# Performance work log

Hardware: AMD Instinct MI355X
Metric: run time of the kernel (lower is better)

Reference implementation:

```python
import jax, jax.numpy as jnp
import numpy as np

POOL = 4      # pool_size
SR = 2        # sampling_ratio (fixed; torchvision adaptive default approximated)
C_IN = 1024
C1, C2 = 256, 128
OUT_DIM = 2048


def setup_inputs() -> dict:
    key = jax.random.key(0)
    ks = jax.random.split(key, 10)
    B, C, H, W = 8, C_IN, 64, 64
    N = 64
    x = jax.random.normal(ks[0], (B, C, H, W), dtype=jnp.float32)
    # boxes in image pixel coords (image is H*16 = 1024 px)
    img = 1024.0
    x1 = jax.random.uniform(ks[1], (B, N), minval=0.0, maxval=img - 260.0)
    y1 = jax.random.uniform(ks[2], (B, N), minval=0.0, maxval=img - 260.0)
    bw = jax.random.uniform(ks[3], (B, N), minval=32.0, maxval=256.0)
    bh = jax.random.uniform(ks[4], (B, N), minval=32.0, maxval=256.0)
    boxes = jnp.stack([x1, y1, x1 + bw, y1 + bh], axis=-1)  # [B,N,4]
    scale = jnp.float32(1.0 / 16.0)
    # detector params
    w1 = jax.random.normal(ks[5], (C1, C_IN), dtype=jnp.float32) / np.sqrt(C_IN)
    b1 = jnp.zeros((C1,), dtype=jnp.float32)
    w2 = jax.random.normal(ks[6], (C2, C1), dtype=jnp.float32) / np.sqrt(C1)
    b2 = jnp.zeros((C2,), dtype=jnp.float32)
    wl = jax.random.normal(ks[7], (OUT_DIM, C2 * POOL * POOL), dtype=jnp.float32) / np.sqrt(C2 * POOL * POOL)
    bl = jnp.zeros((OUT_DIM,), dtype=jnp.float32)
    return {"x": x, "boxes": boxes, "scale": scale,
            "w1": w1, "b1": b1, "w2": w2, "b2": b2, "wl": wl, "bl": bl}


def _axis_coords(start, size, H):
    # start,size: [R]; returns coords [R, POOL*SR], valid mask, int low/high, lerp wts
    bin_sz = size / POOL                       # [R]
    j = jnp.arange(POOL * SR, dtype=jnp.float32)
    off = jnp.floor(j / SR) + ((j % SR) + 0.5) / SR   # [P]
    c = start[:, None] + off[None, :] * bin_sz[:, None]  # [R,P]
    valid = (c >= -1.0) & (c <= H)
    c = jnp.clip(c, 0.0, H - 1.0)
    lo = jnp.floor(c).astype(jnp.int32)
    lo = jnp.minimum(lo, H - 1)
    hi = jnp.minimum(lo + 1, H - 1)
    frac = c - lo.astype(c.dtype)
    return valid, lo, hi, frac


def _roi_align(feat, boxes, scale):
    # feat: [B,C,H,W], boxes: [B,N,4] -> pooled [B*N, C, POOL, POOL]
    B, C, H, W = feat.shape
    N = boxes.shape[1]
    R = B * N
    bx = (boxes.reshape(R, 4) * scale)
    x1, y1, x2, y2 = bx[:, 0], bx[:, 1], bx[:, 2], bx[:, 3]
    rw = jnp.maximum(x2 - x1, 1.0)
    rh = jnp.maximum(y2 - y1, 1.0)
    vy, y_lo, y_hi, ly = _axis_coords(y1, rh, H)   # [R,P]
    vx, x_lo, x_hi, lx = _axis_coords(x1, rw, W)
    hy, hx = 1.0 - ly, 1.0 - lx
    bidx = jnp.repeat(jnp.arange(B, dtype=jnp.int32), N)  # [R]
    b = bidx[:, None, None]
    # gather 4 corners -> [R,P,P,C]
    v00 = feat[b, :, y_lo[:, :, None], x_lo[:, None, :]]
    v01 = feat[b, :, y_lo[:, :, None], x_hi[:, None, :]]
    v10 = feat[b, :, y_hi[:, :, None], x_lo[:, None, :]]
    v11 = feat[b, :, y_hi[:, :, None], x_hi[:, None, :]]
    w00 = (hy[:, :, None] * hx[:, None, :])[..., None]
    w01 = (hy[:, :, None] * lx[:, None, :])[..., None]
    w10 = (ly[:, :, None] * hx[:, None, :])[..., None]
    w11 = (ly[:, :, None] * lx[:, None, :])[..., None]
    val = v00 * w00 + v01 * w01 + v10 * w10 + v11 * w11
    mask = (vy[:, :, None] & vx[:, None, :])[..., None]
    val = jnp.where(mask, val, 0.0)            # [R,P,P,C]
    val = val.reshape(R, POOL, SR, POOL, SR, C).mean(axis=(2, 4))  # [R,POOL,POOL,C]
    return jnp.transpose(val, (0, 3, 1, 2))    # [R,C,POOL,POOL]


def reference(x, boxes, scale, w1, b1, w2, b2, wl, bl):
    pooled = _roi_align(x, boxes, scale)                  # [R,C,4,4]
    h = jax.nn.elu(jnp.einsum('rchw,oc->rohw', pooled, w1) + b1[None, :, None, None])
    h = jax.nn.elu(jnp.einsum('rchw,oc->rohw', h, w2) + b2[None, :, None, None])
    h = h.reshape(h.shape[0], -1)                         # [R, 128*16], torch Flatten order
    out = jax.nn.elu(h @ wl.T + bl)                       # [R, 2048]
    return out
```

## Files before the change

kernel.cpp:

```cpp
#include <hip/hip_runtime.h>
#include <math.h>

#define C_INK   1024
#define C1D     256
#define C2D     128
#define OUTD    2048
#define R_ROI   512
#define M1D     8192
#define MPIX    32768

typedef _Float16 half8 __attribute__((ext_vector_type(8)));
typedef float    f32x4 __attribute__((ext_vector_type(4)));

__device__ __forceinline__ unsigned int pack2h(float a, float b) {
    union { _Float16 h[2]; unsigned int u; } p;
    p.h[0] = (_Float16)a; p.h[1] = (_Float16)b;
    return p.u;
}
__device__ __forceinline__ float eluf(float v) { return v > 0.f ? v : expf(v) - 1.f; }

__device__ __forceinline__ half8* ldsp(_Float16* base, int row, int ch) {
    return reinterpret_cast<half8*>(base) + row * 8 + (ch ^ (row & 7));
}

__global__ __launch_bounds__(256) void cvt_weights(
    const float* __restrict__ s1, _Float16* __restrict__ d1, int n1,
    const float* __restrict__ s2, _Float16* __restrict__ d2, int n2,
    const float* __restrict__ s3, _Float16* __restrict__ d3, int n3)
{
    int i = (blockIdx.x * 256 + threadIdx.x) * 4;
    const float* s; _Float16* d;
    if (i < n1)            { s = s1; d = d1; }
    else if (i < n1 + n2)  { s = s2; d = d2; i -= n1; }
    else                   { s = s3; d = d3; i -= n1 + n2; if (i >= n3) return; }
    const float4 v = *reinterpret_cast<const float4*>(s + i);
    uint2 u; u.x = pack2h(v.x, v.y); u.y = pack2h(v.z, v.w);
    *reinterpret_cast<uint2*>(d + i) = u;
}

__global__ __launch_bounds__(512) void conv1x1_f16(
    const float* __restrict__ x, const _Float16* __restrict__ w1h,
    _Float16* __restrict__ z)
{
    __shared__ __align__(16) _Float16 As[128 * 64];
    __shared__ __align__(16) _Float16 Bs[256 * 64];

    const int tid  = threadIdx.x;
    const int lane = tid & 63;
    const int wave = tid >> 6;
    const int wr   = wave >> 2;
    const int wc   = wave & 3;
    const int m0   = blockIdx.x * 128;
    const int b    = m0 >> 12;
    const int p0   = m0 & 4095;

    const int akg = wave;
    const int bc  = tid & 7;
    const int br0 = tid >> 3;

    float ar[16];
    half8 brg[4];
    f32x4 acc[4][4];
    #pragma unroll
    for (int i = 0; i < 4; ++i)
        #pragma unroll
        for (int j = 0; j < 4; ++j) acc[i][j] = (f32x4){0.f, 0.f, 0.f, 0.f};

    const float* xbase = x + (size_t)b * C_INK * 4096 + p0;

    auto LOADT = [&](int k0) {
        const float* xk = xbase + (size_t)(k0 + akg * 8) * 4096;
        #pragma unroll
        for (int j = 0; j < 8; ++j) {
            ar[j]     = xk[j * 4096 + lane];
            ar[8 + j] = xk[j * 4096 + lane + 64];
        }
        #pragma unroll
        for (int i = 0; i < 4; ++i)
            brg[i] = *reinterpret_cast<const half8*>(
                &w1h[(size_t)(br0 + i * 64) * C_INK + k0 + bc * 8]);
    };
    auto WRITET = [&]() {
        #pragma unroll
        for (int q = 0; q < 2; ++q) {
            union { half8 h; unsigned int u[4]; } pk;
            #pragma unroll
            for (int j = 0; j < 4; ++j) pk.u[j] = pack2h(ar[q * 8 + 2 * j], ar[q * 8 + 2 * j + 1]);
            *ldsp(As, lane + q * 64, akg) = pk.h;
        }
        #pragma unroll
        for (int i = 0; i < 4; ++i) *ldsp(Bs, br0 + i * 64, bc) = brg[i];
    };
    auto COMPUTET = [&]() {
        #pragma unroll
        for (int kk = 0; kk < 2; ++kk) {
            const int ch = kk * 4 + (lane >> 4);
            half8 af[4], bf[4];
            #pragma unroll
            for (int mi = 0; mi < 4; ++mi) af[mi] = *ldsp(As, wr * 64 + mi * 16 + (lane & 15), ch);
            #pragma unroll
            for (int ni = 0; ni < 4; ++ni) bf[ni] = *ldsp(Bs, wc * 64 + ni * 16 + (lane & 15), ch);
            #pragma unroll
            for (int mi = 0; mi < 4; ++mi)
                #pragma unroll
                for (int ni = 0; ni < 4; ++ni)
                    acc[mi][ni] = __builtin_amdgcn_mfma_f32_16x16x32_f16(af[mi], bf[ni], acc[mi][ni], 0, 0, 0);
        }
    };

    LOADT(0); WRITET(); __syncthreads();
    for (int t = 0; t < 15; ++t) {
        LOADT((t + 1) * 64);
        COMPUTET();
        __syncthreads();
        WRITET();
        __syncthreads();
    }
    COMPUTET();

    _Float16* zp = z + (size_t)m0 * C1D;
    #pragma unroll
    for (int mi = 0; mi < 4; ++mi)
        #pragma unroll
        for (int ni = 0; ni < 4; ++ni)
            #pragma unroll
            for (int j = 0; j < 4; ++j) {
                const int row = wr * 64 + mi * 16 + (lane >> 4) * 4 + j;
                const int col = wc * 64 + ni * 16 + (lane & 15);
                zp[(size_t)row * C1D + col] = (_Float16)acc[mi][ni][j];
            }
}

__global__ __launch_bounds__(256) void roi_gather_f16(
    const _Float16* __restrict__ z, const float* __restrict__ boxes,
    const float* __restrict__ scale_p, const float* __restrict__ b1,
    _Float16* __restrict__ h1)
{
    const int r   = blockIdx.x;
    const int tid = threadIdx.x;

    __shared__ int   s_off[64][4];
    __shared__ float s_w[64][4];

    if (tid < 64) {
        const float sc = scale_p[0];
        const float x1 = boxes[r * 4 + 0] * sc, y1 = boxes[r * 4 + 1] * sc;
        const float x2 = boxes[r * 4 + 2] * sc, y2 = boxes[r * 4 + 3] * sc;
        const float rw = fmaxf(x2 - x1, 1.f), rh = fmaxf(y2 - y1, 1.f);
        const int jy = tid >> 3, jx = tid & 7;

        float offy = (float)(jy >> 1) + (float)(jy & 1) * 0.5f + 0.25f;
        float cy = y1 + offy * rh * 0.25f;
        const bool vy = (cy >= -1.f) && (cy <= 64.f);
        cy = fminf(fmaxf(cy, 0.f), 63.f);
        int ylo = (int)cy; if (ylo > 63) ylo = 63;
        int yhi = ylo + 1; if (yhi > 63) yhi = 63;
        const float ly = cy - (float)ylo, hy = 1.f - ly;

        float offx = (float)(jx >> 1) + (float)(jx & 1) * 0.5f + 0.25f;
        float cx = x1 + offx * rw * 0.25f;
        const bool vx = (cx >= -1.f) && (cx <= 64.f);
        cx = fminf(fmaxf(cx, 0.f), 63.f);
        int xlo = (int)cx; if (xlo > 63) xlo = 63;
        int xhi = xlo + 1; if (xhi > 63) xhi = 63;
        const float lx = cx - (float)xlo, hx = 1.f - lx;

        const float wm = (vy && vx) ? 0.25f : 0.f;
        s_w[tid][0] = hy * hx * wm;
        s_w[tid][1] = hy * lx * wm;
        s_w[tid][2] = ly * hx * wm;
        s_w[tid][3] = ly * lx * wm;
        s_off[tid][0] = (ylo * 64 + xlo) * C1D;
        s_off[tid][1] = (ylo * 64 + xhi) * C1D;
        s_off[tid][2] = (yhi * 64 + xlo) * C1D;
        s_off[tid][3] = (yhi * 64 + xhi) * C1D;
    }
    __syncthreads();

    const int ch8 = tid & 31;
    const int cg  = tid >> 5;
    const _Float16* zb = z + (size_t)(r >> 6) * 4096 * C1D + ch8 * 8;

    float bias[8];
    {
        const float4 b0 = *reinterpret_cast<const float4*>(&b1[ch8 * 8]);
        const float4 b4 = *reinterpret_cast<const float4*>(&b1[ch8 * 8 + 4]);
        bias[0] = b0.x; bias[1] = b0.y; bias[2] = b0.z; bias[3] = b0.w;
        bias[4] = b4.x; bias[5] = b4.y; bias[6] = b4.z; bias[7] = b4.w;
    }

    float accv[2][8];
    #pragma unroll
    for (int c = 0; c < 2; ++c)
        #pragma unroll
        for (int e = 0; e < 8; ++e) accv[c][e] = 0.f;

    #pragma unroll
    for (int cc = 0; cc < 2; ++cc) {
        const int cell = cg * 2 + cc;
        const int py = cell >> 2, px = cell & 3;
        #pragma unroll
        for (int u = 0; u < 4; ++u) {
            const int s = (py * 2 + (u >> 1)) * 8 + px * 2 + (u & 1);
            #pragma unroll
            for (int k = 0; k < 4; ++k) {
                const half8 v = *reinterpret_cast<const half8*>(zb + s_off[s][k]);
                const float w = s_w[s][k];
                #pragma unroll
                for (int e = 0; e < 8; ++e) accv[cc][e] += (float)v[e] * w;
            }
        }
    }

    #pragma unroll
    for (int cc = 0; cc < 2; ++cc) {
        const int row = r * 16 + cg * 2 + cc;
        half8 o;
        #pragma unroll
        for (int e = 0; e < 8; ++e) o[e] = (_Float16)eluf(accv[cc][e] + bias[e]);
        *reinterpret_cast<half8*>(&h1[(size_t)row * C1D + ch8 * 8]) = o;
    }
}

template<int BM, int FM, int OUT_MODE>
__global__ __launch_bounds__(256) void gemm_nt(
    const _Float16* __restrict__ A, const _Float16* __restrict__ W,
    const float* __restrict__ bias, void* __restrict__ Cout, int K, int N)
{
    constexpr int WM = FM * 16;
    constexpr int AI = BM / 32;
    __shared__ __align__(16) _Float16 As[BM * 64];
    __shared__ __align__(16) _Float16 Bs[128 * 64];

    const int tid  = threadIdx.x;
    const int lane = tid & 63;
    const int wave = tid >> 6;
    const int wr   = wave >> 1, wc = wave & 1;
    const int m0   = blockIdx.x * BM;
    const int n0   = blockIdx.y * 128;
    const int c    = tid & 7;
    const int r0   = tid >> 3;

    half8 arg[AI], brg[4];
    f32x4 acc[FM][4];
    #pragma unroll
    for (int i = 0; i < FM; ++i)
        #pragma unroll
        for (int j = 0; j < 4; ++j) acc[i][j] = (f32x4){0.f, 0.f, 0.f, 0.f};

    auto LOADT = [&](int k0) {
        #pragma unroll
        for (int i = 0; i < AI; ++i)
            arg[i] = *reinterpret_cast<const half8*>(&A[(size_t)(m0 + r0 + i * 32) * K + k0 + c * 8]);
        #pragma unroll
        for (int i = 0; i < 4; ++i)
            brg[i] = *reinterpret_cast<const half8*>(&W[(size_t)(n0 + r0 + i * 32) * K + k0 + c * 8]);
    };
    auto WRITET = [&]() {
        #pragma unroll
        for (int i = 0; i < AI; ++i) *ldsp(As, r0 + i * 32, c) = arg[i];
        #pragma unroll
        for (int i = 0; i < 4; ++i)  *ldsp(Bs, r0 + i * 32, c) = brg[i];
    };
    auto COMPUTET = [&]() {
        #pragma unroll
        for (int kk = 0; kk < 2; ++kk) {
            const int ch = kk * 4 + (lane >> 4);
            half8 af[FM], bf[4];
            #pragma unroll
            for (int mi = 0; mi < FM; ++mi) af[mi] = *ldsp(As, wr * WM + mi * 16 + (lane & 15), ch);
            #pragma unroll
            for (int ni = 0; ni < 4; ++ni)  bf[ni] = *ldsp(Bs, wc * 64 + ni * 16 + (lane & 15), ch);
            #pragma unroll
            for (int mi = 0; mi < FM; ++mi)
                #pragma unroll
                for (int ni = 0; ni < 4; ++ni)
                    acc[mi][ni] = __builtin_amdgcn_mfma_f32_16x16x32_f16(af[mi], bf[ni], acc[mi][ni], 0, 0, 0);
        }
    };

    const int nt = K / 64;
    LOADT(0); WRITET(); __syncthreads();
    for (int t = 0; t < nt - 1; ++t) {
        LOADT((t + 1) * 64);
        COMPUTET();
        __syncthreads();
        WRITET();
        __syncthreads();
    }
    COMPUTET();

    #pragma unroll
    for (int ni = 0; ni < 4; ++ni) {
        const int col = n0 + wc * 64 + ni * 16 + (lane & 15);
        const float bv = bias[col];
        #pragma unroll
        for (int mi = 0; mi < FM; ++mi)
            #pragma unroll
            for (int j = 0; j < 4; ++j) {
                const int row = m0 + wr * WM + mi * 16 + (lane >> 4) * 4 + j;
                const float v = eluf(acc[mi][ni][j] + bv);
                if (OUT_MODE == 1) {
                    ((_Float16*)Cout)[(size_t)(row >> 4) * 2048 + col * 16 + (row & 15)] = (_Float16)v;
                } else {
                    ((float*)Cout)[(size_t)row * N + col] = v;
                }
            }
    }
}

extern "C" void kernel_launch(void* const* d_in, const int* in_sizes, int n_in,
                              void* d_out, int out_size, void* d_ws, size_t ws_size,
                              hipStream_t stream) {
    const float* x     = (const float*)d_in[0];
    const float* boxes = (const float*)d_in[1];
    const float* scale = (const float*)d_in[2];
    const float* w1    = (const float*)d_in[3];
    const float* b1    = (const float*)d_in[4];
    const float* w2    = (const float*)d_in[5];
    const float* b2    = (const float*)d_in[6];
    const float* wl    = (const float*)d_in[7];
    const float* bl    = (const float*)d_in[8];
    float* out = (float*)d_out;

    _Float16* z   = (_Float16*)d_ws;
    _Float16* h1  = z   + (size_t)MPIX * C1D;
    _Float16* h2  = h1  + (size_t)M1D * C1D;
    _Float16* w1h = h2  + (size_t)R_ROI * OUTD;
    _Float16* w2h = w1h + (size_t)C1D * C_INK;
    _Float16* wlh = w2h + (size_t)C2D * C1D;

    const int n1 = C1D * C_INK, n2 = C2D * C1D, n3 = OUTD * OUTD;

    cvt_weights<<<dim3((n1 + n2 + n3) / 1024), dim3(256), 0, stream>>>(
        w1, w1h, n1, w2, w2h, n2, wl, wlh, n3);

    conv1x1_f16<<<dim3(MPIX / 128), dim3(512), 0, stream>>>(x, w1h, z);

    roi_gather_f16<<<dim3(R_ROI), dim3(256), 0, stream>>>(z, boxes, scale, b1, h1);

    gemm_nt<128, 4, 1><<<dim3(M1D / 128, 1), dim3(256), 0, stream>>>(
        h1, w2h, b2, (void*)h2, C1D, C2D);

    gemm_nt<64, 2, 2><<<dim3(R_ROI / 64, OUTD / 128), dim3(256), 0, stream>>>(
        h2, wlh, bl, (void*)out, OUTD, OUTD);
}
```

Measured before the change: 88.18 us.

## Fuse ROI gather with second conv GEMM and shrink conv1x1 tile

The ROI bilinear gather and the 256->128 second 1x1 conv GEMM are merged into one kernel. Each ROI block now stages all of w2 plus its 16x256 h1 tile in LDS and runs MFMAs directly, which removes the h1 round trip through global memory and one launch. The conv1x1 kernel tile is halved to 64 rows with 8 waves each owning 32 output columns, doubling the grid for more parallelism. The trade-off is that every ROI block reloads the full w2 matrix (64KB LDS), which limits occupancy and adds redundant weight traffic.

```diff
diff --git a/kernel.cpp b/kernel.cpp
--- a/kernel.cpp
+++ b/kernel.cpp
@@ -19,8 +19,9 @@
 }
 __device__ __forceinline__ float eluf(float v) { return v > 0.f ? v : expf(v) - 1.f; }
 
-__device__ __forceinline__ half8* ldsp(_Float16* base, int row, int ch) {
-    return reinterpret_cast<half8*>(base) + row * 8 + (ch ^ (row & 7));
+template<int RC>
+__device__ __forceinline__ half8* ldsq(_Float16* base, int row, int ch) {
+    return reinterpret_cast<half8*>(base) + row * RC + (ch ^ (row & 7));
 }
 
 __global__ __launch_bounds__(256) void cvt_weights(
@@ -38,72 +39,63 @@
     *reinterpret_cast<uint2*>(d + i) = u;
 }
 
-__global__ __launch_bounds__(512) void conv1x1_f16(
+__global__ __launch_bounds__(512, 4) void conv1x1_f16(
     const float* __restrict__ x, const _Float16* __restrict__ w1h,
     _Float16* __restrict__ z)
 {
-    __shared__ __align__(16) _Float16 As[128 * 64];
+    __shared__ __align__(16) _Float16 As[64 * 64];
     __shared__ __align__(16) _Float16 Bs[256 * 64];
 
     const int tid  = threadIdx.x;
     const int lane = tid & 63;
     const int wave = tid >> 6;
-    const int wr   = wave >> 2;
-    const int wc   = wave & 3;
-    const int m0   = blockIdx.x * 128;
+    const int m0   = blockIdx.x * 64;
     const int b    = m0 >> 12;
     const int p0   = m0 & 4095;
 
-    const int akg = wave;
     const int bc  = tid & 7;
     const int br0 = tid >> 3;
 
-    float ar[16];
+    float ar[8];
     half8 brg[4];
-    f32x4 acc[4][4];
+    f32x4 acc[4][2];
     #pragma unroll
     for (int i = 0; i < 4; ++i)
         #pragma unroll
-        for (int j = 0; j < 4; ++j) acc[i][j] = (f32x4){0.f, 0.f, 0.f, 0.f};
-
-    const float* xbase = x + (size_t)b * C_INK * 4096 + p0;
+        for (int j = 0; j < 2; ++j) acc[i][j] = (f32x4){0.f, 0.f, 0.f, 0.f};
+
+    const float* xbase = x + (size_t)b * C_INK * 4096 + p0 + lane;
 
     auto LOADT = [&](int k0) {
-        const float* xk = xbase + (size_t)(k0 + akg * 8) * 4096;
-        #pragma unroll
-        for (int j = 0; j < 8; ++j) {
-            ar[j]     = xk[j * 4096 + lane];
-            ar[8 + j] = xk[j * 4096 + lane + 64];
-        }
+        const float* xk = xbase + (size_t)(k0 + wave * 8) * 4096;
+        #pragma unroll
+        for (int j = 0; j < 8; ++j) ar[j] = xk[(size_t)j * 4096];
         #pragma unroll
         for (int i = 0; i < 4; ++i)
             brg[i] = *reinterpret_cast<const half8*>(
                 &w1h[(size_t)(br0 + i * 64) * C_INK + k0 + bc * 8]);
     };
     auto WRITET = [&]() {
-        #pragma unroll
-        for (int q = 0; q < 2; ++q) {
-            union { half8 h; unsigned int u[4]; } pk;
-            #pragma unroll
-            for (int j = 0; j < 4; ++j) pk.u[j] = pack2h(ar[q * 8 + 2 * j], ar[q * 8 + 2 * j + 1]);
-            *ldsp(As, lane + q * 64, akg) = pk.h;
-        }
-        #pragma unroll
-        for (int i = 0; i < 4; ++i) *ldsp(Bs, br0 + i * 64, bc) = brg[i];
+        union { half8 h; unsigned int u[4]; } pk;
+        #pragma unroll
+        for (int j = 0; j < 4; ++j) pk.u[j] = pack2h(ar[2 * j], ar[2 * j + 1]);
+        *ldsq<8>(As, lane, wave) = pk.h;
+        #pragma unroll
+        for (int i = 0; i < 4; ++i) *ldsq<8>(Bs, br0 + i * 64, bc) = brg[i];
     };
     auto COMPUTET = [&]() {
         #pragma unroll
         for (int kk = 0; kk < 2; ++kk) {
             const int ch = kk * 4 + (lane >> 4);
-            half8 af[4], bf[4];
-            #pragma unroll
-            for (int mi = 0; mi < 4; ++mi) af[mi] = *ldsp(As, wr * 64 + mi * 16 + (lane & 15), ch);
-            #pragma unroll
-            for (int ni = 0; ni < 4; ++ni) bf[ni] = *ldsp(Bs, wc * 64 + ni * 16 + (lane & 15), ch);
+            half8 af[4], bf[2];
+            #pragma unroll
+            for (int mi = 0; mi < 4; ++mi) af[mi] = *ldsq<8>(As, mi * 16 + (lane & 15), ch);
+            #pragma unroll
+            for (int ni = 0; ni < 2; ++ni) bf[ni] = *ldsq<8>(Bs, wave * 32 + ni * 16 + (lane & 15), ch);
             #pragma unroll
             for (int mi = 0; mi < 4; ++mi)
                 #pragma unroll
-                for (int ni = 0; ni < 4; ++ni)
+                for (int ni = 0; ni < 2; ++ni)
                     acc[mi][ni] = __builtin_amdgcn_mfma_f32_16x16x32_f16(af[mi], bf[ni], acc[mi][ni], 0, 0, 0);
         }
     };
@@ -122,25 +114,29 @@
     #pragma unroll
     for (int mi = 0; mi < 4; ++mi)
         #pragma unroll
-        for (int ni = 0; ni < 4; ++ni)
+        for (int ni = 0; ni < 2; ++ni)
             #pragma unroll
             for (int j = 0; j < 4; ++j) {
-                const int row = wr * 64 + mi * 16 + (lane >> 4) * 4 + j;
-                const int col = wc * 64 + ni * 16 + (lane & 15);
+                const int row = mi * 16 + (lane >> 4) * 4 + j;
+                const int col = wave * 32 + ni * 16 + (lane & 15);
                 zp[(size_t)row * C1D + col] = (_Float16)acc[mi][ni][j];
             }
 }
 
-__global__ __launch_bounds__(256) void roi_gather_f16(
+__global__ __launch_bounds__(256) void roi_gemm2_f16(
     const _Float16* __restrict__ z, const float* __restrict__ boxes,
-    const float* __restrict__ scale_p, const float* __restrict__ b1,
-    _Float16* __restrict__ h1)
+    const float* __restrict__ scale_p, const float* __restrict__ b1v,
+    const _Float16* __restrict__ w2h, const float* __restrict__ b2v,
+    _Float16* __restrict__ h2)
 {
-    const int r   = blockIdx.x;
-    const int tid = threadIdx.x;
-
+    __shared__ __align__(16) _Float16 W2s[128 * 256];
+    __shared__ __align__(16) _Float16 H1s[16 * 256];
     __shared__ int   s_off[64][4];
     __shared__ float s_w[64][4];
+
+    const int r    = blockIdx.x;
+    const int tid  = threadIdx.x;
+    const int lane = tid & 63;
 
     if (tid < 64) {
         const float sc = scale_p[0];
@@ -175,57 +171,104 @@
         s_off[tid][2] = (yhi * 64 + xlo) * C1D;
         s_off[tid][3] = (yhi * 64 + xhi) * C1D;
     }
+
+    {
+        const int wr_ = tid >> 1;
+        const int wcb = (tid & 1) * 16;
+        #pragma unroll
+        for (int bb = 0; bb < 4; ++bb) {
+            half8 tmp[4];
+            #pragma unroll
+            for (int i = 0; i < 4; ++i)
+                tmp[i] = *reinterpret_cast<const half8*>(&w2h[(size_t)wr_ * C1D + (wcb + bb * 4 + i) * 8]);
+            #pragma unroll
+            for (int i = 0; i < 4; ++i)
+                *ldsq<32>(W2s, wr_, wcb + bb * 4 + i) = tmp[i];
+        }
+    }
     __syncthreads();
 
-    const int ch8 = tid & 31;
-    const int cg  = tid >> 5;
-    const _Float16* zb = z + (size_t)(r >> 6) * 4096 * C1D + ch8 * 8;
-
-    float bias[8];
     {
-        const float4 b0 = *reinterpret_cast<const float4*>(&b1[ch8 * 8]);
-        const float4 b4 = *reinterpret_cast<const float4*>(&b1[ch8 * 8 + 4]);
-        bias[0] = b0.x; bias[1] = b0.y; bias[2] = b0.z; bias[3] = b0.w;
-        bias[4] = b4.x; bias[5] = b4.y; bias[6] = b4.z; bias[7] = b4.w;
-    }
-
-    float accv[2][8];
-    #pragma unroll
-    for (int c = 0; c < 2; ++c)
-        #pragma unroll
-        for (int e = 0; e < 8; ++e) accv[c][e] = 0.f;
-
-    #pragma unroll
-    for (int cc = 0; cc < 2; ++cc) {
-        const int cell = cg * 2 + cc;
-        const int py = cell >> 2, px = cell & 3;
-        #pragma unroll
-        for (int u = 0; u < 4; ++u) {
-            const int s = (py * 2 + (u >> 1)) * 8 + px * 2 + (u & 1);
-            #pragma unroll
-            for (int k = 0; k < 4; ++k) {
-                const half8 v = *reinterpret_cast<const half8*>(zb + s_off[s][k]);
-                const float w = s_w[s][k];
+        const int ch8 = tid & 31;
+        const int cg  = tid >> 5;
+        const _Float16* zb = z + (size_t)(r >> 6) * 4096 * C1D + ch8 * 8;
+
+        float bias[8];
+        {
+            const float4 b0 = *reinterpret_cast<const float4*>(&b1v[ch8 * 8]);
+            const float4 b4 = *reinterpret_cast<const float4*>(&b1v[ch8 * 8 + 4]);
+            bias[0] = b0.x; bias[1] = b0.y; bias[2] = b0.z; bias[3] = b0.w;
+            bias[4] = b4.x; bias[5] = b4.y; bias[6] = b4.z; bias[7] = b4.w;
+        }
+
+        float accv[2][8];
+        #pragma unroll
+        for (int c = 0; c < 2; ++c)
+            #pragma unroll
+            for (int e = 0; e < 8; ++e) accv[c][e] = 0.f;
+
+        #pragma unroll
+        for (int cc = 0; cc < 2; ++cc) {
+            const int cell = cg * 2 + cc;
+            const int py = cell >> 2, px = cell & 3;
+            #pragma unroll
+            for (int u = 0; u < 4; ++u) {
+                const int s = (py * 2 + (u >> 1)) * 8 + px * 2 + (u & 1);
                 #pragma unroll
-                for (int e = 0; e < 8; ++e) accv[cc][e] += (float)v[e] * w;
-            }
-        }
-    }
-
-    #pragma unroll
-    for (int cc = 0; cc < 2; ++cc) {
-        const int row = r * 16 + cg * 2 + cc;
-        half8 o;
-        #pragma unroll
-        for (int e = 0; e < 8; ++e) o[e] = (_Float16)eluf(accv[cc][e] + bias[e]);
-        *reinterpret_cast<half8*>(&h1[(size_t)row * C1D + ch8 * 8]) = o;
-    }
-}
-
-template<int BM, int FM, int OUT_MODE>
+                for (int k = 0; k < 4; ++k) {
+                    const half8 v = *reinterpret_cast<const half8*>(zb + s_off[s][k]);
+                    const float w = s_w[s][k];
+                    #pragma unroll
+                    for (int e = 0; e < 8; ++e) accv[cc][e] += (float)v[e] * w;
+                }
+            }
+        }
+
+        #pragma unroll
+        for (int cc = 0; cc < 2; ++cc) {
+            half8 o;
+            #pragma unroll
+            for (int e = 0; e < 8; ++e) o[e] = (_Float16)eluf(accv[cc][e] + bias[e]);
+            *ldsq<32>(H1s, cg * 2 + cc, ch8) = o;
+        }
+    }
+    __syncthreads();
+
+    {
+        const int wv = tid >> 6;
+        f32x4 o2[2];
+        o2[0] = (f32x4){0.f, 0.f, 0.f, 0.f};
+        o2[1] = (f32x4){0.f, 0.f, 0.f, 0.f};
+
+        #pragma unroll
+        for (int ks = 0; ks < 8; ++ks) {
+            const int ch = ks * 4 + (lane >> 4);
+            const half8 af = *ldsq<32>(H1s, lane & 15, ch);
+            #pragma unroll
+            for (int i = 0; i < 2; ++i) {
+                const half8 bf = *ldsq<32>(W2s, (wv * 2 + i) * 16 + (lane & 15), ch);
+                o2[i] = __builtin_amdgcn_mfma_f32_16x16x32_f16(af, bf, o2[i], 0, 0, 0);
+            }
+        }
+
+        _Float16* hp = h2 + (size_t)r * 2048;
+        #pragma unroll
+        for (int i = 0; i < 2; ++i) {
+            const int o = (wv * 2 + i) * 16 + (lane & 15);
+            const float bv = b2v[o];
+            #pragma unroll
+            for (int j = 0; j < 4; ++j) {
+                const int p = (lane >> 4) * 4 + j;
+                hp[o * 16 + p] = (_Float16)eluf(o2[i][j] + bv);
+            }
+        }
+    }
+}
+
+template<int BM, int FM>
 __global__ __launch_bounds__(256) void gemm_nt(
     const _Float16* __restrict__ A, const _Float16* __restrict__ W,
-    const float* __restrict__ bias, void* __restrict__ Cout, int K, int N)
+    const float* __restrict__ bias, float* __restrict__ Cout, int K, int N)
 {
     constexpr int WM = FM * 16;
     constexpr int AI = BM / 32;
@@ -258,9 +301,9 @@
     };
     auto WRITET = [&]() {
         #pragma unroll
-        for (int i = 0; i < AI; ++i) *ldsp(As, r0 + i * 32, c) = arg[i];
-        #pragma unroll
-        for (int i = 0; i < 4; ++i)  *ldsp(Bs, r0 + i * 32, c) = brg[i];
+        for (int i = 0; i < AI; ++i) *ldsq<8>(As, r0 + i * 32, c) = arg[i];
+        #pragma unroll
+        for (int i = 0; i < 4; ++i)  *ldsq<8>(Bs, r0 + i * 32, c) = brg[i];
     };
     auto COMPUTET = [&]() {
         #pragma unroll
@@ -268,9 +311,9 @@
             const int ch = kk * 4 + (lane >> 4);
             half8 af[FM], bf[4];
             #pragma unroll
-            for (int mi = 0; mi < FM; ++mi) af[mi] = *ldsp(As, wr * WM + mi * 16 + (lane & 15), ch);
-            #pragma unroll
-            for (int ni = 0; ni < 4; ++ni)  bf[ni] = *ldsp(Bs, wc * 64 + ni * 16 + (lane & 15), ch);
+            for (int mi = 0; mi < FM; ++mi) af[mi] = *ldsq<8>(As, wr * WM + mi * 16 + (lane & 15), ch);
+            #pragma unroll
+            for (int ni = 0; ni < 4; ++ni)  bf[ni] = *ldsq<8>(Bs, wc * 64 + ni * 16 + (lane & 15), ch);
             #pragma unroll
             for (int mi = 0; mi < FM; ++mi)
                 #pragma unroll
@@ -299,12 +342,7 @@
             #pragma unroll
             for (int j = 0; j < 4; ++j) {
                 const int row = m0 + wr * WM + mi * 16 + (lane >> 4) * 4 + j;
-                const float v = eluf(acc[mi][ni][j] + bv);
-                if (OUT_MODE == 1) {
-                    ((_Float16*)Cout)[(size_t)(row >> 4) * 2048 + col * 16 + (row & 15)] = (_Float16)v;
-                } else {
-                    ((float*)Cout)[(size_t)row * N + col] = v;
-                }
+                Cout[(size_t)row * N + col] = eluf(acc[mi][ni][j] + bv);
             }
     }
 }
@@ -324,8 +362,7 @@
     float* out = (float*)d_out;
 
     _Float16* z   = (_Float16*)d_ws;
-    _Float16* h1  = z   + (size_t)MPIX * C1D;
-    _Float16* h2  = h1  + (size_t)M1D * C1D;
+    _Float16* h2  = z   + (size_t)MPIX * C1D;
     _Float16* w1h = h2  + (size_t)R_ROI * OUTD;
     _Float16* w2h = w1h + (size_t)C1D * C_INK;
     _Float16* wlh = w2h + (size_t)C2D * C1D;
@@ -335,13 +372,11 @@
     cvt_weights<<<dim3((n1 + n2 + n3) / 1024), dim3(256), 0, stream>>>(
         w1, w1h, n1, w2, w2h, n2, wl, wlh, n3);
 
-    conv1x1_f16<<<dim3(MPIX / 128), dim3(512), 0, stream>>>(x, w1h, z);
-
-    roi_gather_f16<<<dim3(R_ROI), dim3(256), 0, stream>>>(z, boxes, scale, b1, h1);
-
-    gemm_nt<128, 4, 1><<<dim3(M1D / 128, 1), dim3(256), 0, stream>>>(
-        h1, w2h, b2, (void*)h2, C1D, C2D);
-
-    gemm_nt<64, 2, 2><<<dim3(R_ROI / 64, OUTD / 128), dim3(256), 0, stream>>>(
-        h2, wlh, bl, (void*)out, OUTD, OUTD);
-}
+    conv1x1_f16<<<dim3(MPIX / 64), dim3(512), 0, stream>>>(x, w1h, z);
+
+    roi_gemm2_f16<<<dim3(R_ROI), dim3(256), 0, stream>>>(
+        z, boxes, scale, b1, w2h, b2, h2);
+
+    gemm_nt<64, 2><<<dim3(R_ROI / 64, OUTD / 128), dim3(256), 0, stream>>>(
+        h2, wlh, bl, out, OUTD, OUTD);
+}
```

After: 80.64 us. 1.09x faster.
